# Optimization experiments

Hardware: AMD Instinct MI355X
Metric: run time of the kernel (lower is better)

The kernel has to match this reference:

```python
import jax, jax.numpy as jnp
import numpy as np

KAPPA = 5  # kNN neighbors per node (module hardcodes kappas = [5]*B, topk of KAPPA+2)


def build_graph(inputs):
    """Vectorized equivalent of get_graph(): returns flat (src, dst, edge_weight)
    over the B*S node space. Filtered kNN edges (dst < 2) are masked via weight 0,
    which is mathematically identical to removing them (gcn_norm uses edge weights)."""
    B, S, _ = inputs.shape
    diff = inputs[:, :, None, :] - inputs[:, None, :, :]            # [B,S,S,2]
    deltas = jnp.sqrt(jnp.sum(diff * diff, axis=-1))                # torch.cdist
    eye = jnp.eye(S, dtype=bool)
    d = jnp.where(eye[None], jnp.inf, deltas)                       # fill_diagonal_(inf)
    nodes = jnp.arange(2, S, dtype=jnp.int32)                       # non-depot nodes
    # depot edges: 0 -> i  and  i -> 1  for i in [2, S)
    src_dep = jnp.concatenate([jnp.zeros(S - 2, jnp.int32), nodes])
    dst_dep = jnp.concatenate([nodes, jnp.ones(S - 2, jnp.int32)])
    # kNN edges: 7 nearest per non-depot node (diag=inf so i never selected)
    _, idx = jax.lax.top_k(-d[:, 2:, :], KAPPA + 2)                 # [B, S-2, 7]
    src_knn = jnp.broadcast_to(nodes[:, None], (S - 2, KAPPA + 2)).reshape(-1)
    dst_knn = idx.reshape(B, -1).astype(jnp.int32)                  # [B, 7*(S-2)]
    mask_knn = (dst_knn >= 2).astype(jnp.float32)                   # drop depot dsts
    src = jnp.concatenate([jnp.broadcast_to(src_dep[None], (B, src_dep.shape[0])), jnp.broadcast_to(src_knn[None], (B, src_knn.shape[0]))], axis=1)
    dst = jnp.concatenate([jnp.broadcast_to(dst_dep[None], (B, dst_dep.shape[0])), dst_knn], axis=1)
    ew = jnp.concatenate([jnp.ones((B, dst_dep.shape[0]), jnp.float32), mask_knn], axis=1)
    offs = (jnp.arange(B, dtype=jnp.int32) * S)[:, None]            # batch node offset
    return (src + offs).reshape(-1), (dst + offs).reshape(-1), ew.reshape(-1)


def gcn_conv(x, src, dst, norm, self_norm, W, b, N):
    h = x @ W                                                       # GCNConv linear
    agg = jax.ops.segment_sum(h[src] * norm[:, None], dst, num_segments=N)
    agg = agg + h * self_norm[:, None]                              # self-loop term
    return agg + b


def gnn_forward(x, src, dst, ew, W0, b0, W1, b1, W2, b2):
    N = x.shape[0]
    deg = jax.ops.segment_sum(ew, dst, num_segments=N) + 1.0        # +1 self-loop
    dinv = 1.0 / jnp.sqrt(deg)
    norm = dinv[src] * dinv[dst] * ew                               # sym gcn_norm
    self_norm = dinv * dinv
    h = jax.nn.relu(gcn_conv(x, src, dst, norm, self_norm, W0, b0, N))
    h = jax.nn.relu(gcn_conv(h, src, dst, norm, self_norm, W1, b1, N))
    return gcn_conv(h, src, dst, norm, self_norm, W2, b2, N)


def setup_inputs() -> dict:
    B, S, D, H = 64, 1000, 128, 512
    key = jax.random.key(0)
    ks = jax.random.split(key, 12)
    sc = lambda fan_in: 1.0 / np.sqrt(fan_in)
    return {
        "inputs": jax.random.uniform(ks[0], (B, S, 2), jnp.float32),
        "scor": jax.random.uniform(ks[1], (B, S, 1), jnp.float32),
        "Wc": jax.random.normal(ks[2], (2, D), jnp.float32) * sc(2),
        "bc": jax.random.normal(ks[3], (D,), jnp.float32) * 0.01,
        "Ws": jax.random.normal(ks[4], (1, D), jnp.float32) * sc(1),
        "bs": jax.random.normal(ks[5], (D,), jnp.float32) * 0.01,
        "W0": jax.random.normal(ks[6], (D, H), jnp.float32) * sc(D),
        "b0": jnp.zeros((H,), jnp.float32),
        "W1": jax.random.normal(ks[8], (H, H), jnp.float32) * sc(H),
        "b1": jnp.zeros((H,), jnp.float32),
        "W2": jax.random.normal(ks[10], (H, D), jnp.float32) * sc(H),
        "b2": jnp.zeros((D,), jnp.float32),
    }


def reference(inputs, scor, Wc, bc, Ws, bs, W0, b0, W1, b1, W2, b2):
    B, S, _ = inputs.shape
    src, dst, ew = build_graph(inputs)
    x = (inputs @ Wc + bc) + (scor @ Ws + bs)                       # embedded_data
    x = x.reshape(B * S, -1)
    out = gnn_forward(x, src, dst, ew, W0, b0, W1, b1, W2, b2)
    return out.reshape(B, S, -1)
```

## Files before the change

kernel.cpp:

```cpp
#include <hip/hip_runtime.h>

typedef unsigned short u16;
typedef unsigned int u32;
typedef unsigned long long u64;
using short8 = __attribute__((ext_vector_type(8))) short;
using f32x4  = __attribute__((ext_vector_type(4))) float;

constexpr int Bb = 64, Ss = 1000, Dd = 128, Hh = 512;
constexpr int NN = Bb * Ss;
constexpr int NSRC = Ss - 2;

__device__ __forceinline__ float bf2f(u16 h) {
    u32 u = ((u32)h) << 16;
    return __builtin_bit_cast(float, u);
}
__device__ __forceinline__ u16 f2bf(float v) {
    u32 u = __builtin_bit_cast(u32, v);
    u32 r = (u + 0x7FFFu + ((u >> 16) & 1u)) >> 16;
    return (u16)r;
}
__device__ __forceinline__ float4 bf4(ushort4 v) {
    float4 r;
    r.x = bf2f(v.x); r.y = bf2f(v.y); r.z = bf2f(v.z); r.w = bf2f(v.w);
    return r;
}
__device__ __forceinline__ void gl_lds16(const void* g, void* l) {
    __builtin_amdgcn_global_load_lds(
        (const __attribute__((address_space(1))) void*)g,
        (__attribute__((address_space(3))) void*)l, 16, 0, 0);
}
__device__ __forceinline__ void acc8(float (&a)[8], uint4 v, float w) {
    u32 c[4] = {v.x, v.y, v.z, v.w};
#pragma unroll
    for (int k = 0; k < 4; ++k) {
        float lo = __builtin_bit_cast(float, c[k] << 16);
        float hi = __builtin_bit_cast(float, c[k] & 0xFFFF0000u);
        a[2 * k]     += lo * w;
        a[2 * k + 1] += hi * w;
    }
}
__device__ __forceinline__ void acc2(float (&a)[2], u32 v, float w) {
    float lo = __builtin_bit_cast(float, v << 16);
    float hi = __builtin_bit_cast(float, v & 0xFFFF0000u);
    a[0] += lo * w;
    a[1] += hi * w;
}
__device__ __forceinline__ void unp8(float (&a)[8], uint4 v) {
    u32 c[4] = {v.x, v.y, v.z, v.w};
#pragma unroll
    for (int k = 0; k < 4; ++k) {
        a[2 * k]     = __builtin_bit_cast(float, c[k] << 16);
        a[2 * k + 1] = __builtin_bit_cast(float, c[k] & 0xFFFF0000u);
    }
}

__device__ __forceinline__ u64 umin64(u64 a, u64 b) { return a < b ? a : b; }
__device__ __forceinline__ u64 umax64(u64 a, u64 b) { return a < b ? b : a; }

__device__ __forceinline__ void ins8u(u64 (&bd)[8], u64 v) {
#pragma unroll
    for (int k = 7; k >= 1; --k)
        bd[k] = umin64(umax64(v, bd[k - 1]), bd[k]);
    bd[0] = umin64(v, bd[0]);
}

__device__ __forceinline__ void merge8(u64 (&a)[8], int mask) {
    u64 b[8];
#pragma unroll
    for (int k = 0; k < 8; ++k)
        b[k] = __shfl_xor((unsigned long long)a[k], mask);
    u64 m[8];
#pragma unroll
    for (int k = 0; k < 8; ++k) m[k] = umin64(a[k], b[7 - k]);
#pragma unroll
    for (int k = 0; k < 4; ++k) {
        u64 lo = umin64(m[k], m[k + 4]), hi = umax64(m[k], m[k + 4]);
        m[k] = lo; m[k + 4] = hi;
    }
#pragma unroll
    for (int base = 0; base < 8; base += 4)
#pragma unroll
        for (int k = 0; k < 2; ++k) {
            u64 lo = umin64(m[base + k], m[base + k + 2]);
            u64 hi = umax64(m[base + k], m[base + k + 2]);
            m[base + k] = lo; m[base + k + 2] = hi;
        }
#pragma unroll
    for (int base = 0; base < 8; base += 2) {
        u64 lo = umin64(m[base], m[base + 1]), hi = umax64(m[base], m[base + 1]);
        m[base] = lo; m[base + 1] = hi;
    }
#pragma unroll
    for (int k = 0; k < 8; ++k) a[k] = m[k];
}

__global__ __launch_bounds__(256) void knn_bin_kernel(const float* __restrict__ inputs,
                                                      float2* __restrict__ gsxy,
                                                      u16* __restrict__ gsid,
                                                      int* __restrict__ gcst) {
    __shared__ float px[Ss], py[Ss];
    __shared__ int hist[256];
    __shared__ int cur[256];
    int b = blockIdx.x;
    int tid = threadIdx.x;
    const float* base = inputs + (size_t)b * Ss * 2;
    for (int t = tid; t < Ss; t += 256) { px[t] = base[2 * t]; py[t] = base[2 * t + 1]; }
    hist[tid] = 0;
    __syncthreads();
    for (int t = tid; t < Ss; t += 256) {
        int cx = min(15, (int)(px[t] * 16.0f));
        int cy = min(15, (int)(py[t] * 16.0f));
        atomicAdd(&hist[cy * 16 + cx], 1);
    }
    __syncthreads();
    int cnt = hist[tid];
    for (int s = 1; s < 256; s <<= 1) {
        int u = (tid >= s) ? hist[tid - s] : 0;
        __syncthreads();
        hist[tid] += u;
        __syncthreads();
    }
    int st = hist[tid] - cnt;
    cur[tid] = st;
    gcst[b * 260 + tid] = st;
    if (tid == 0) gcst[b * 260 + 256] = Ss;
    __syncthreads();
    for (int t = tid; t < Ss; t += 256) {
        float x = px[t], y = py[t];
        int cx = min(15, (int)(x * 16.0f));
        int cy = min(15, (int)(y * 16.0f));
        int p = atomicAdd(&cur[cy * 16 + cx], 1);
        gsxy[b * 1000 + p] = make_float2(x, y);
        gsid[b * 1000 + p] = (u16)t;
    }
}

__global__ __launch_bounds__(256) void knn_query_kernel(const float* __restrict__ inputs,
                                                        const float2* __restrict__ gsxy,
                                                        const u16* __restrict__ gsid,
                                                        const int* __restrict__ gcst,
                                                        u16* __restrict__ knn,
                                                        int* __restrict__ indeg) {
    __shared__ float2 sxy[Ss];
    __shared__ u16 sid[Ss];
    __shared__ int cst[257];
    int b = blockIdx.x;
    int tid = threadIdx.x;
    for (int t = tid; t < Ss; t += 256) { sxy[t] = gsxy[b * 1000 + t]; sid[t] = gsid[b * 1000 + t]; }
    for (int t = tid; t < 257; t += 256) cst[t] = gcst[b * 260 + t];
    __syncthreads();

    int sub = tid & 7;
    int g = tid >> 3;
    int i = 2 + blockIdx.y * 32 + g;
    if (i >= Ss) return;

    float x = inputs[(size_t)b * 2000 + 2 * i];
    float y = inputs[(size_t)b * 2000 + 2 * i + 1];
    int cx = min(15, (int)(x * 16.0f));
    int cy = min(15, (int)(y * 16.0f));
    const float INF = __builtin_inff();
    constexpr float h = 0.0625f;

    u64 bd[8];
    int w = 1;
    for (;;) {
#pragma unroll
        for (int k = 0; k < 8; ++k) bd[k] = ~0ULL;
        int x0 = max(0, cx - w), x1 = min(15, cx + w);
        int y0 = max(0, cy - w), y1 = min(15, cy + w);
        for (int cyy = y0; cyy <= y1; ++cyy) {
            int p0 = cst[cyy * 16 + x0];
            int p1 = cst[cyy * 16 + x1 + 1];
            for (int p = p0 + sub; p < p1; p += 8) {
                float2 q = sxy[p];
                int j = sid[p];
                float dx = __fsub_rn(x, q.x);
                float dy = __fsub_rn(y, q.y);
                float d2 = __fadd_rn(__fmul_rn(dx, dx), __fmul_rn(dy, dy));
                float d = __fsqrt_rn(d2);
                u64 key = (((u64)__builtin_bit_cast(u32, d)) << 32) | (u32)j;
                key = (j == i) ? ~0ULL : key;
                ins8u(bd, key);
            }
        }
        merge8(bd, 1); merge8(bd, 2); merge8(bd, 4);
        float d7 = __builtin_bit_cast(float, (u32)(bd[6] >> 32));
        float bL = (x0 > 0)  ? (x - (float)x0 * h) : INF;
        float bR = (x1 < 15) ? ((float)(x1 + 1) * h - x) : INF;
        float bB = (y0 > 0)  ? (y - (float)y0 * h) : INF;
        float bT = (y1 < 15) ? ((float)(y1 + 1) * h - y) : INF;
        float bound = fminf(fminf(bL, bR), fminf(bB, bT));
        if (d7 <= bound - 2e-6f || w >= 16) break;
        ++w;
    }

    if (sub == 0) {
        u16* kp = knn + ((size_t)b * NSRC + (i - 2)) * 7;
#pragma unroll
        for (int k = 0; k < 7; ++k) {
            int j = (int)(u32)bd[k];
            kp[k] = (u16)j;
            if (j >= 2) atomicAdd(&indeg[b * Ss + j], 1);
        }
    }
}

__global__ __launch_bounds__(1024) void scan1_kernel(const int* __restrict__ indeg,
                                                     int* __restrict__ offs,
                                                     int* __restrict__ bsum,
                                                     float* __restrict__ dinv) {
    __shared__ int sh[1024];
    int t = threadIdx.x;
    int idx = blockIdx.x * 1024 + t;
    int v = (idx < NN) ? indeg[idx] : 0;
    sh[t] = v;
    __syncthreads();
    for (int off = 1; off < 1024; off <<= 1) {
        int u = (t >= off) ? sh[t - off] : 0;
        __syncthreads();
        sh[t] += u;
        __syncthreads();
    }
    if (idx < NN) {
        offs[idx] = sh[t] - v;
        int ii = idx % Ss;
        float deg = (ii == 0) ? 1.0f : (ii == 1) ? (float)(Ss - 1) : (float)(v + 2);
        dinv[idx] = 1.0f / __fsqrt_rn(deg);
    }
    if (t == 1023) bsum[blockIdx.x] = sh[1023];
}

__global__ void scan2_kernel(int* __restrict__ bsum) {
    if (threadIdx.x == 0) {
        int run = 0;
        for (int k = 0; k < 63; ++k) { int v = bsum[k]; bsum[k] = run; run += v; }
        bsum[63] = run;
    }
}

__global__ __launch_bounds__(1024) void scan3_kernel(int* __restrict__ offs,
                                                     const int* __restrict__ bsum) {
    int idx = blockIdx.x * 1024 + threadIdx.x;
    if (idx < NN) offs[idx] += bsum[blockIdx.x];
    if (idx == 0) offs[NN] = bsum[63];
}

__global__ __launch_bounds__(256) void fill_rev_kernel(const u16* __restrict__ knn,
                                                       const int* __restrict__ offs,
                                                       int* __restrict__ cursor,
                                                       u16* __restrict__ rev) {
    if (threadIdx.x >= 250) return;
    int b = blockIdx.x;
    int i = 2 + blockIdx.y * 250 + threadIdx.x;
    if (i >= Ss) return;
    const u16* kp = knn + ((size_t)b * NSRC + (i - 2)) * 7;
#pragma unroll
    for (int k = 0; k < 7; ++k) {
        int d = kp[k];
        if (d >= 2) {
            int n = b * Ss + d;
            int p = atomicAdd(&cursor[n], 1);
            rev[offs[n] + p] = (u16)i;
        }
    }
}

__global__ __launch_bounds__(512) void fuse0_kernel(const float* __restrict__ Wc,
                                                    const float* __restrict__ bc,
                                                    const float* __restrict__ Ws,
                                                    const float* __restrict__ bs,
                                                    const float* __restrict__ W0,
                                                    float* __restrict__ A) {
    int h = threadIdx.x;
    float a0 = 0.f, a1 = 0.f, a2 = 0.f, a3 = 0.f;
    for (int c = 0; c < Dd; ++c) {
        float w = W0[c * Hh + h];
        a0 += Wc[c] * w;
        a1 += Wc[Dd + c] * w;
        a2 += Ws[c] * w;
        a3 += (bc[c] + bs[c]) * w;
    }
    A[h] = a0; A[Hh + h] = a1; A[2 * Hh + h] = a2; A[3 * Hh + h] = a3;
}

__global__ __launch_bounds__(1024) void agg_e_kernel(const float* __restrict__ inputs,
                                                     const float* __restrict__ scor,
                                                     const float* __restrict__ dinv,
                                                     const int* __restrict__ offs,
                                                     const int* __restrict__ indeg,
                                                     const u16* __restrict__ rev,
                                                     float4* __restrict__ ve) {
    __shared__ float se0[Ss], se1[Ss], se2[Ss], sdv[Ss];
    __shared__ float4 depw[16];
    int b = blockIdx.x;
    int tid = threadIdx.x;
    int nb = b * Ss;
    const float* base = inputs + (size_t)nb * 2;
    for (int t = tid; t < Ss; t += 1024) {
        se0[t] = base[2 * t];
        se1[t] = base[2 * t + 1];
        se2[t] = scor[nb + t];
        sdv[t] = dinv[nb + t];
    }
    __syncthreads();

    float4 dep = {0.f, 0.f, 0.f, 0.f};
    for (int r = tid; r < Ss; r += 1024) {
        if (r >= 2) {
            float w = sdv[r];
            dep.x += se0[r] * w; dep.y += se1[r] * w;
            dep.z += se2[r] * w; dep.w += w;
        }
    }
#pragma unroll
    for (int m = 1; m < 64; m <<= 1) {
        dep.x += __shfl_xor(dep.x, m);
        dep.y += __shfl_xor(dep.y, m);
        dep.z += __shfl_xor(dep.z, m);
        dep.w += __shfl_xor(dep.w, m);
    }
    if ((tid & 63) == 0) depw[tid >> 6] = dep;
    __syncthreads();

    int i = tid;
    if (i >= Ss) return;
    float dn = sdv[i], sn = dn * dn;
    float4 acc = {0.f, 0.f, 0.f, 0.f};
    if (i >= 2) {
        int n = nb + i;
        int cnt = indeg[n], o = offs[n];
        float w0 = sdv[0];
        acc.x = se0[0] * w0; acc.y = se1[0] * w0;
        acc.z = se2[0] * w0; acc.w = w0;
        for (int e = 0; e < cnt; ++e) {
            int s = rev[o + e];
            float w = sdv[s];
            acc.x += se0[s] * w; acc.y += se1[s] * w;
            acc.z += se2[s] * w; acc.w += w;
        }
    } else if (i == 1) {
        float4 t = {0.f, 0.f, 0.f, 0.f};
#pragma unroll
        for (int k = 0; k < 16; ++k) {
            t.x += depw[k].x; t.y += depw[k].y;
            t.z += depw[k].z; t.w += depw[k].w;
        }
        acc = t;
    }
    float4 v;
    v.x = acc.x * dn + se0[i] * sn;
    v.y = acc.y * dn + se1[i] * sn;
    v.z = acc.z * dn + se2[i] * sn;
    v.w = acc.w * dn + sn;
    ve[nb + i] = v;
}

__global__ __launch_bounds__(256) void expand512p_kernel(const float4* __restrict__ ve,
                                                         const float* __restrict__ dinv,
                                                         const float* __restrict__ A,
                                                         const float* __restrict__ bias,
                                                         u16* __restrict__ X,
                                                         float* __restrict__ sxp) {
    __shared__ float4 sve[250];
    __shared__ float  sdv[250];
    __shared__ float  sred[8][256];
    int bx = blockIdx.x;
    int g = bx >> 1, cg = bx & 1;
    int b = blockIdx.y;
    int n0 = g * 250;
    int nb = b * Ss;
    int tid = threadIdx.x;
    int c32 = tid & 31, slice = tid >> 5;
    int ch = cg * 256 + c32 * 8;
    for (int t = tid; t < 250; t += 256) {
        sve[t] = ve[nb + n0 + t];
        sdv[t] = dinv[nb + n0 + t];
    }
    __syncthreads();

    float A0[8], A1[8], A2[8], A3[8], BZ[8];
#pragma unroll
    for (int j = 0; j < 8; ++j) {
        A0[j] = A[ch + j];
        A1[j] = A[Hh + ch + j];
        A2[j] = A[2 * Hh + ch + j];
        A3[j] = A[3 * Hh + ch + j];
        BZ[j] = bias[ch + j];
    }
    float acc[8] = {};
    for (int t = slice; t < 250; t += 8) {
        int n = n0 + t;
        float4 v = sve[t];
        float dw = (n >= 2) ? sdv[t] : 0.f;
        u32 ow[4];
#pragma unroll
        for (int j = 0; j < 4; ++j) {
            float z0 = fmaxf(v.x * A0[2 * j]     + v.y * A1[2 * j]     + v.z * A2[2 * j]     + v.w * A3[2 * j]     + BZ[2 * j],     0.f);
            float z1 = fmaxf(v.x * A0[2 * j + 1] + v.y * A1[2 * j + 1] + v.z * A2[2 * j + 1] + v.w * A3[2 * j + 1] + BZ[2 * j + 1], 0.f);
            u16 h0 = f2bf(z0), h1 = f2bf(z1);
            ow[j] = (u32)h0 | ((u32)h1 << 16);
            acc[2 * j]     += dw * bf2f(h0);
            acc[2 * j + 1] += dw * bf2f(h1);
        }
        uint4 o = {ow[0], ow[1], ow[2], ow[3]};
        *(uint4*)(X + (size_t)(nb + n) * Hh + ch) = o;
    }
#pragma unroll
    for (int j = 0; j < 8; ++j) sred[slice][c32 * 8 + j] = acc[j];
    __syncthreads();
    if (slice == 0) {
#pragma unroll
        for (int j = 0; j < 8; ++j) {
            float s = 0.f;
#pragma unroll
            for (int sl = 0; sl < 8; ++sl) s += sred[sl][c32 * 8 + j];
            sxp[((size_t)b * 4 + g) * Hh + ch + j] = s;
        }
    }
}

__global__ __launch_bounds__(512) void sxk_kernel(const float* __restrict__ sxp,
                                                  const float* __restrict__ W1,
                                                  float* __restrict__ depp) {
    __shared__ float sx[64];
    int kc = blockIdx.x;
    int b  = blockIdx.y;
    int t  = threadIdx.x;
    if (t < 64) {
        int k = kc * 64 + t;
        float s = 0.f;
#pragma unroll
        for (int g = 0; g < 4; ++g) s += sxp[((size_t)b * 4 + g) * Hh + k];
        sx[t] = s;
    }
    __syncthreads();
    float a = 0.f;
#pragma unroll 8
    for (int kk = 0; kk < 64; ++kk)
        a += sx[kk] * W1[(size_t)(kc * 64 + kk) * Hh + t];
    depp[((size_t)kc * Bb + b) * Hh + t] = a;
}

__global__ __launch_bounds__(512) void sxred_kernel(const float* __restrict__ depp,
                                                    float* __restrict__ depf) {
    int b = blockIdx.x, t = threadIdx.x;
    float s = 0.f;
#pragma unroll
    for (int kc = 0; kc < 8; ++kc)
        s += depp[((size_t)kc * Bb + b) * Hh + t];
    depf[(size_t)b * Hh + t] = s;
}

__global__ void transp_kernel(const float* __restrict__ src,
                              u16* __restrict__ dst, int R, int C) {
    int gid = blockIdx.x * 256 + threadIdx.x;
    if (gid >= R * C) return;
    int r = gid / C, c = gid - r * C;
    dst[c * R + r] = f2bf(src[gid]);
}

__global__ __launch_bounds__(256) void gemm_kernel(const u16* __restrict__ A,
                                                   const u16* __restrict__ W,
                                                   u16* __restrict__ Y,
                                                   int K, int Ncols,
                                                   int nyb, int nxb) {
    __shared__ __align__(16) u16 lA[128][64];
    __shared__ __align__(16) u16 lW[128][64];

    int grp = blockIdx.x / (8 * nxb);
    int rem = blockIdx.x - grp * (8 * nxb);
    int xcd = rem & 7;
    int xb  = rem >> 3;
    int yb  = grp * 8 + xcd;
    if (yb >= nyb) return;

    int row0 = yb * 128;
    int col0 = xb * 128;
    int tid = threadIdx.x;
    int lane = tid & 63, wid = tid >> 6;
    int wm = (wid >> 1) * 64, wn = (wid & 1) * 64;
    int lanelo = lane & 15, quad = lane >> 4;

    int lrow = lane >> 3;
    int lslot = lane & 7;

    f32x4 acc[4][4] = {};

    for (int k0 = 0; k0 < K; k0 += 64) {
#pragma unroll
        for (int t = 0; t < 4; ++t) {
            int chunk = t * 4 + wid;
            int row = chunk * 8 + lrow;
            int sc = lslot ^ (row & 7);
            gl_lds16(A + (size_t)(row0 + row) * K + k0 + sc * 8, &lA[chunk * 8][0]);
        }
#pragma unroll
        for (int t = 0; t < 4; ++t) {
            int chunk = t * 4 + wid;
            int row = chunk * 8 + lrow;
            int sc = lslot ^ (row & 7);
            gl_lds16(W + (size_t)(col0 + row) * K + k0 + sc * 8, &lW[chunk * 8][0]);
        }
        __syncthreads();

#pragma unroll
        for (int kk = 0; kk < 64; kk += 32) {
            short8 af[4], bw[4];
            int cbb = (kk >> 3) + quad;
#pragma unroll
            for (int mt = 0; mt < 4; ++mt) {
                int r = wm + mt * 16 + lanelo;
                af[mt] = *(const short8*)&lA[r][((cbb ^ (r & 7))) * 8];
            }
#pragma unroll
            for (int nt = 0; nt < 4; ++nt) {
                int r = wn + nt * 16 + lanelo;
                bw[nt] = *(const short8*)&lW[r][((cbb ^ (r & 7))) * 8];
            }
#pragma unroll
            for (int mt = 0; mt < 4; ++mt)
#pragma unroll
                for (int nt = 0; nt < 4; ++nt)
                    acc[mt][nt] = __builtin_amdgcn_mfma_f32_16x16x32_bf16(
                        af[mt], bw[nt], acc[mt][nt], 0, 0, 0);
        }
        __syncthreads();
    }

#pragma unroll
    for (int mt = 0; mt < 4; ++mt)
#pragma unroll
        for (int nt = 0; nt < 4; ++nt)
#pragma unroll
            for (int r = 0; r < 4; ++r) {
                int row = row0 + wm + mt * 16 + quad * 4 + r;
                int col = col0 + wn + nt * 16 + lanelo;
                Y[(size_t)row * Ncols + col] = f2bf(acc[mt][nt][r]);
            }
}

__global__ __launch_bounds__(1024) void dep1_kernel(const u16* __restrict__ y,
                                                    const float* __restrict__ dinv,
                                                    float* __restrict__ dq,
                                                    int M) {
    int b = blockIdx.x;
    int qq = blockIdx.y;
    int co = blockIdx.z * 128;
    int tid = threadIdx.x;
    int c4 = tid & 31;
    int es = tid >> 5;
    int j0 = 2 + qq * 250;
    int j1 = j0 + 250; if (j1 > Ss) j1 = Ss;
    const u16* yb = y + (size_t)b * Ss * M + co + c4 * 4;
    const float* dv = dinv + b * Ss;
    float a0 = 0.f, a1 = 0.f, a2 = 0.f, a3 = 0.f;
    for (int j = j0 + es; j < j1; j += 32) {
        float w = dv[j];
        float4 u = bf4(*(const ushort4*)(yb + (size_t)j * M));
        a0 += u.x * w; a1 += u.y * w; a2 += u.z * w; a3 += u.w * w;
    }
    __shared__ float4 red[1024];
    float4 mv; mv.x = a0; mv.y = a1; mv.z = a2; mv.w = a3;
    red[tid] = mv;
    __syncthreads();
#pragma unroll
    for (int s = 16; s > 0; s >>= 1) {
        if (es < s) {
            float4 o = red[tid + (s << 5)];
            float4 m = red[tid];
            m.x += o.x; m.y += o.y; m.z += o.z; m.w += o.w;
            red[tid] = m;
        }
        __syncthreads();
    }
    if (es == 0)
        *(float4*)(dq + ((size_t)qq * Bb + b) * M + co + c4 * 4) = red[c4];
}

__global__ __launch_bounds__(256) void aggw512_kernel(const u16* __restrict__ y,
                                                      const float* __restrict__ dinv,
                                                      const int* __restrict__ offs,
                                                      const int* __restrict__ indeg,
                                                      const u16* __restrict__ rev,
                                                      const float* __restrict__ bias,
                                                      const float* __restrict__ dep1,
                                                      u16* __restrict__ oX) {
    int tid = threadIdx.x;
    int wv = tid >> 6, lane = tid & 63;
    int bx = blockIdx.x;
    int b = (bx & 7) + 8 * (bx / 2000);
    int i = ((bx >> 3) % 250) * 4 + wv;
    int nb = b * Ss;
    int n = nb + i;
    const u16* yB = y + (size_t)nb * 512 + lane * 8;

    float acc[8] = {};
    if (i >= 2) {
        int cnt = indeg[n], o = offs[n];
        int rv = 0; float rw = 0.f;
        if (lane < 16 && lane < cnt) { rv = rev[o + lane]; rw = dinv[nb + rv]; }
        float w0 = dinv[nb];
        uint4 v0 = *(const uint4*)yB;
        acc8(acc, v0, w0);
        int cl = cnt < 16 ? cnt : 16;
        int e = 0;
        for (; e + 4 <= cl; e += 4) {
            int   s0 = __shfl(rv, e),     s1 = __shfl(rv, e + 1);
            int   s2 = __shfl(rv, e + 2), s3 = __shfl(rv, e + 3);
            float w_0 = __shfl(rw, e),     w_1 = __shfl(rw, e + 1);
            float w_2 = __shfl(rw, e + 2), w_3 = __shfl(rw, e + 3);
            uint4 u0 = *(const uint4*)(yB + (size_t)s0 * 512);
            uint4 u1 = *(const uint4*)(yB + (size_t)s1 * 512);
            uint4 u2 = *(const uint4*)(yB + (size_t)s2 * 512);
            uint4 u3 = *(const uint4*)(yB + (size_t)s3 * 512);
            acc8(acc, u0, w_0); acc8(acc, u1, w_1);
            acc8(acc, u2, w_2); acc8(acc, u3, w_3);
        }
        for (; e < cl; ++e) {
            int s = __shfl(rv, e); float ww = __shfl(rw, e);
            uint4 u = *(const uint4*)(yB + (size_t)s * 512);
            acc8(acc, u, ww);
        }
        for (; e < cnt; ++e) {
            int s = rev[o + e]; float ww = dinv[nb + s];
            uint4 u = *(const uint4*)(yB + (size_t)s * 512);
            acc8(acc, u, ww);
        }
    } else if (i == 1) {
        const float* dp = dep1 + (size_t)b * 512 + lane * 8;
        float4 v0 = *(const float4*)dp;
        float4 v1 = *(const float4*)(dp + 4);
        acc[0] = v0.x; acc[1] = v0.y; acc[2] = v0.z; acc[3] = v0.w;
        acc[4] = v1.x; acc[5] = v1.y; acc[6] = v1.z; acc[7] = v1.w;
    }
    float dn = dinv[n], sn = dn * dn;
    float s8[8];
    unp8(s8, *(const uint4*)(yB + (size_t)i * 512));
    float4 bl = *(const float4*)(bias + lane * 8);
    float4 bh = *(const float4*)(bias + lane * 8 + 4);
    float bz[8] = {bl.x, bl.y, bl.z, bl.w, bh.x, bh.y, bh.z, bh.w};
    u32 ow[4];
#pragma unroll
    for (int k = 0; k < 4; ++k) {
        float z0 = acc[2 * k]     * dn + s8[2 * k]     * sn + bz[2 * k];
        float z1 = acc[2 * k + 1] * dn + s8[2 * k + 1] * sn + bz[2 * k + 1];
        ow[k] = (u32)f2bf(fmaxf(z0, 0.f)) | ((u32)f2bf(fmaxf(z1, 0.f)) << 16);
    }
    uint4 ov = {ow[0], ow[1], ow[2], ow[3]};
    *(uint4*)(oX + (size_t)n * 512 + lane * 8) = ov;
}

__global__ __launch_bounds__(256) void aggwf128_kernel(const u16* __restrict__ y,
                                                       const float* __restrict__ dinv,
                                                       const int* __restrict__ offs,
                                                       const int* __restrict__ indeg,
                                                       const u16* __restrict__ rev,
                                                       const float* __restrict__ bias,
                                                       const float* __restrict__ dep1,
                                                       float* __restrict__ out) {
    int tid = threadIdx.x;
    int wv = tid >> 6, lane = tid & 63;
    int bx = blockIdx.x;
    int b = (bx & 7) + 8 * (bx / 2000);
    int i = ((bx >> 3) % 250) * 4 + wv;
    int nb = b * Ss;
    int n = nb + i;
    const u16* yB = y + (size_t)nb * 128 + lane * 2;

    float acc[2] = {};
    if (i >= 2) {
        int cnt = indeg[n], o = offs[n];
        int rv = 0; float rw = 0.f;
        if (lane < 16 && lane < cnt) { rv = rev[o + lane]; rw = dinv[nb + rv]; }
        float w0 = dinv[nb];
        acc2(acc, *(const u32*)yB, w0);
        int cl = cnt < 16 ? cnt : 16;
        int e = 0;
        for (; e + 4 <= cl; e += 4) {
            int   s0 = __shfl(rv, e),     s1 = __shfl(rv, e + 1);
            int   s2 = __shfl(rv, e + 2), s3 = __shfl(rv, e + 3);
            float w_0 = __shfl(rw, e),     w_1 = __shfl(rw, e + 1);
            float w_2 = __shfl(rw, e + 2), w_3 = __shfl(rw, e + 3);
            u32 u0 = *(const u32*)(yB + (size_t)s0 * 128);
            u32 u1 = *(const u32*)(yB + (size_t)s1 * 128);
            u32 u2 = *(const u32*)(yB + (size_t)s2 * 128);
            u32 u3 = *(const u32*)(yB + (size_t)s3 * 128);
            acc2(acc, u0, w_0); acc2(acc, u1, w_1);
            acc2(acc, u2, w_2); acc2(acc, u3, w_3);
        }
        for (; e < cl; ++e) {
            int s = __shfl(rv, e); float ww = __shfl(rw, e);
            acc2(acc, *(const u32*)(yB + (size_t)s * 128), ww);
        }
        for (; e < cnt; ++e) {
            int s = rev[o + e]; float ww = dinv[nb + s];
            acc2(acc, *(const u32*)(yB + (size_t)s * 128), ww);
        }
    } else if (i == 1) {
        const float* dp = dep1 + (size_t)b * 128 + lane * 2;
#pragma unroll
        for (int qq = 0; qq < 4; ++qq) {
            float2 v = *(const float2*)(dp + (size_t)qq * Bb * 128);
            acc[0] += v.x; acc[1] += v.y;
        }
    }
    float dn = dinv[n], sn = dn * dn;
    u32 sv = *(const u32*)(yB + (size_t)i * 128);
    float s0 = __builtin_bit_cast(float, sv << 16);
    float s1 = __builtin_bit_cast(float, sv & 0xFFFF0000u);
    float2 bz = *(const float2*)(bias + lane * 2);
    float2 z;
    z.x = acc[0] * dn + s0 * sn + bz.x;
    z.y = acc[1] * dn + s1 * sn + bz.y;
    *(float2*)(out + (size_t)n * 128 + lane * 2) = z;
}

constexpr size_t O_INDEG  = 0;
constexpr size_t O_CURSOR = 256000;
constexpr size_t O_OFFS   = 512000;
constexpr size_t O_DINV   = 768256;
constexpr size_t O_KNN    = 1024256;
constexpr size_t O_REV    = 1918080;
constexpr size_t O_AMAT   = 2811904;
constexpr size_t O_WT1    = 2942976;
constexpr size_t O_WT2    = 3467264;
constexpr size_t O_X      = 3598336;
constexpr size_t O_Y      = 69134336;
constexpr size_t O_SXP    = 134670336;
constexpr size_t O_DEPF   = 135194624;
constexpr size_t O_BSUM   = 135325696;
constexpr size_t O_GSXY   = O_X;
constexpr size_t O_GSID   = O_X + 512000;
constexpr size_t O_GCST   = O_X + 640000;
constexpr size_t O_VE     = O_Y;
constexpr size_t O_DEPP   = O_Y + 4194304;

extern "C" void kernel_launch(void* const* d_in, const int* in_sizes, int n_in,
                              void* d_out, int out_size, void* d_ws, size_t ws_size,
                              hipStream_t stream) {
    const float* inputs = (const float*)d_in[0];
    const float* scor   = (const float*)d_in[1];
    const float* Wc     = (const float*)d_in[2];
    const float* bc     = (const float*)d_in[3];
    const float* Ws     = (const float*)d_in[4];
    const float* bs     = (const float*)d_in[5];
    const float* W0     = (const float*)d_in[6];
    const float* b0     = (const float*)d_in[7];
    const float* W1     = (const float*)d_in[8];
    const float* b1     = (const float*)d_in[9];
    const float* W2     = (const float*)d_in[10];
    const float* b2     = (const float*)d_in[11];

    char* w = (char*)d_ws;
    int*    indeg  = (int*)(w + O_INDEG);
    int*    cursor = (int*)(w + O_CURSOR);
    int*    offs   = (int*)(w + O_OFFS);
    float*  dinv   = (float*)(w + O_DINV);
    u16*    knn    = (u16*)(w + O_KNN);
    u16*    rev    = (u16*)(w + O_REV);
    float*  amat   = (float*)(w + O_AMAT);
    u16*    wt1    = (u16*)(w + O_WT1);
    u16*    wt2    = (u16*)(w + O_WT2);
    u16*    xbf    = (u16*)(w + O_X);
    u16*    ybf    = (u16*)(w + O_Y);
    float*  sxp    = (float*)(w + O_SXP);
    float*  depf   = (float*)(w + O_DEPF);
    float*  depp   = (float*)(w + O_DEPP);
    int*    bsum   = (int*)(w + O_BSUM);
    float2* gsxy   = (float2*)(w + O_GSXY);
    u16*    gsid   = (u16*)(w + O_GSID);
    int*    gcst   = (int*)(w + O_GCST);
    float4* ve     = (float4*)(w + O_VE);

    hipMemsetAsync(w + O_INDEG, 0, 512000, stream);

    knn_bin_kernel<<<Bb, 256, 0, stream>>>(inputs, gsxy, gsid, gcst);
    knn_query_kernel<<<dim3(Bb, 32), 256, 0, stream>>>(inputs, gsxy, gsid, gcst, knn, indeg);
    scan1_kernel<<<63, 1024, 0, stream>>>(indeg, offs, bsum, dinv);
    scan2_kernel<<<1, 64, 0, stream>>>(bsum);
    scan3_kernel<<<63, 1024, 0, stream>>>(offs, bsum);
    fill_rev_kernel<<<dim3(Bb, 4), 256, 0, stream>>>(knn, offs, cursor, rev);

    fuse0_kernel<<<1, 512, 0, stream>>>(Wc, bc, Ws, bs, W0, amat);
    transp_kernel<<<(Hh * Hh + 255) / 256, 256, 0, stream>>>(W1, wt1, Hh, Hh);
    transp_kernel<<<(Hh * Dd + 255) / 256, 256, 0, stream>>>(W2, wt2, Hh, Dd);

    agg_e_kernel<<<Bb, 1024, 0, stream>>>(inputs, scor, dinv, offs, indeg, rev, ve);
    expand512p_kernel<<<dim3(8, Bb), 256, 0, stream>>>(ve, dinv, amat, b0, xbf, sxp);
    sxk_kernel<<<dim3(8, Bb), 512, 0, stream>>>(sxp, W1, depp);
    sxred_kernel<<<Bb, 512, 0, stream>>>(depp, depf);
    gemm_kernel<<<63 * 32, 256, 0, stream>>>(xbf, wt1, ybf, Hh, Hh, 500, 4);
    aggw512_kernel<<<NN / 4, 256, 0, stream>>>(ybf, dinv, offs, indeg, rev, b1, depf, xbf);
    gemm_kernel<<<63 * 8, 256, 0, stream>>>(xbf, wt2, ybf, Hh, Dd, 500, 1);
    dep1_kernel<<<dim3(Bb, 4, 1), 1024, 0, stream>>>(ybf, dinv, depf, Dd);
    aggwf128_kernel<<<NN / 4, 256, 0, stream>>>(ybf, dinv, offs, indeg, rev, b2, depf, (float*)d_out);
}
```

Before: 308.9 us.

## Fold scan2 into scan3, merge prep kernels, enlarge GEMM tile to 256 rows

Removes the single-thread scan2 launch by having every scan3 block compute its own prefix of the block sums with wavefront shuffles. Merges fuse0 and the two weight-transpose kernels into one prep kernel to cut launch count. Doubles the GEMM M-tile to 256 rows with 512 threads per block, which raises reuse of the weight tile but halves the number of blocks. The wave-to-tile mapping in the unshown compute part must match the new 8-wave layout.

Result: no change. 310.3 us (+0.5%).

```diff
diff --git a/kernel.cpp b/kernel.cpp
--- a/kernel.cpp
+++ b/kernel.cpp
@@ -231,19 +231,25 @@
     if (t == 1023) bsum[blockIdx.x] = sh[1023];
 }
 
-__global__ void scan2_kernel(int* __restrict__ bsum) {
-    if (threadIdx.x == 0) {
-        int run = 0;
-        for (int k = 0; k < 63; ++k) { int v = bsum[k]; bsum[k] = run; run += v; }
-        bsum[63] = run;
-    }
-}
-
 __global__ __launch_bounds__(1024) void scan3_kernel(int* __restrict__ offs,
                                                      const int* __restrict__ bsum) {
-    int idx = blockIdx.x * 1024 + threadIdx.x;
-    if (idx < NN) offs[idx] += bsum[blockIdx.x];
-    if (idx == 0) offs[NN] = bsum[63];
+    __shared__ int spre, stot;
+    int t = threadIdx.x;
+    if (t < 64) {
+        int v = (t < 63) ? bsum[t] : 0;
+        int pre = (t < (int)blockIdx.x) ? v : 0;
+        int tot = v;
+#pragma unroll
+        for (int m = 1; m < 64; m <<= 1) {
+            pre += __shfl_xor(pre, m);
+            tot += __shfl_xor(tot, m);
+        }
+        if (t == 0) { spre = pre; stot = tot; }
+    }
+    __syncthreads();
+    int idx = blockIdx.x * 1024 + t;
+    if (idx < NN) offs[idx] += spre;
+    if (idx == 0) offs[NN] = stot;
 }
 
 __global__ __launch_bounds__(256) void fill_rev_kernel(const u16* __restrict__ knn,
@@ -266,22 +272,38 @@
     }
 }
 
-__global__ __launch_bounds__(512) void fuse0_kernel(const float* __restrict__ Wc,
-                                                    const float* __restrict__ bc,
-                                                    const float* __restrict__ Ws,
-                                                    const float* __restrict__ bs,
-                                                    const float* __restrict__ W0,
-                                                    float* __restrict__ A) {
-    int h = threadIdx.x;
-    float a0 = 0.f, a1 = 0.f, a2 = 0.f, a3 = 0.f;
-    for (int c = 0; c < Dd; ++c) {
-        float w = W0[c * Hh + h];
-        a0 += Wc[c] * w;
-        a1 += Wc[Dd + c] * w;
-        a2 += Ws[c] * w;
-        a3 += (bc[c] + bs[c]) * w;
-    }
-    A[h] = a0; A[Hh + h] = a1; A[2 * Hh + h] = a2; A[3 * Hh + h] = a3;
+__global__ __launch_bounds__(256) void prep_kernel(const float* __restrict__ Wc,
+                                                   const float* __restrict__ bc,
+                                                   const float* __restrict__ Ws,
+                                                   const float* __restrict__ bs,
+                                                   const float* __restrict__ W0,
+                                                   const float* __restrict__ W1,
+                                                   const float* __restrict__ W2,
+                                                   float* __restrict__ A,
+                                                   u16* __restrict__ wt1,
+                                                   u16* __restrict__ wt2) {
+    int bid = blockIdx.x;
+    int tid = threadIdx.x;
+    if (bid < 1024) {
+        int gid = bid * 256 + tid;
+        int r = gid >> 9, c = gid & 511;
+        wt1[(size_t)c * 512 + r] = f2bf(W1[gid]);
+    } else if (bid < 1024 + 256) {
+        int gid = (bid - 1024) * 256 + tid;
+        int r = gid >> 7, c = gid & 127;
+        wt2[(size_t)c * 512 + r] = f2bf(W2[gid]);
+    } else {
+        int h = (bid - 1280) * 256 + tid;
+        float a0 = 0.f, a1 = 0.f, a2 = 0.f, a3 = 0.f;
+        for (int c = 0; c < Dd; ++c) {
+            float w = W0[c * Hh + h];
+            a0 += Wc[c] * w;
+            a1 += Wc[Dd + c] * w;
+            a2 += Ws[c] * w;
+            a3 += (bc[c] + bs[c]) * w;
+        }
+        A[h] = a0; A[Hh + h] = a1; A[2 * Hh + h] = a2; A[3 * Hh + h] = a3;
+    }
 }
 
 __global__ __launch_bounds__(1024) void agg_e_kernel(const float* __restrict__ inputs,
@@ -452,20 +474,12 @@
     depf[(size_t)b * Hh + t] = s;
 }
 
-__global__ void transp_kernel(const float* __restrict__ src,
-                              u16* __restrict__ dst, int R, int C) {
-    int gid = blockIdx.x * 256 + threadIdx.x;
-    if (gid >= R * C) return;
-    int r = gid / C, c = gid - r * C;
-    dst[c * R + r] = f2bf(src[gid]);
-}
-
-__global__ __launch_bounds__(256) void gemm_kernel(const u16* __restrict__ A,
+__global__ __launch_bounds__(512) void gemm_kernel(const u16* __restrict__ A,
                                                    const u16* __restrict__ W,
                                                    u16* __restrict__ Y,
                                                    int K, int Ncols,
                                                    int nyb, int nxb) {
-    __shared__ __align__(16) u16 lA[128][64];
+    __shared__ __align__(16) u16 lA[256][64];
     __shared__ __align__(16) u16 lW[128][64];
 
     int grp = blockIdx.x / (8 * nxb);
@@ -475,7 +489,7 @@
     int yb  = grp * 8 + xcd;
     if (yb >= nyb) return;
 
-    int row0 = yb * 128;
+    int row0 = yb * 256;
     int col0 = xb * 128;
     int tid = threadIdx.x;
     int lane = tid & 63, wid = tid >> 6;
@@ -490,14 +504,14 @@
     for (int k0 = 0; k0 < K; k0 += 64) {
 #pragma unroll
         for (int t = 0; t < 4; ++t) {
-            int chunk = t * 4 + wid;
+            int chunk = t * 8 + wid;
             int row = chunk * 8 + lrow;
             int sc = lslot ^ (row & 7);
             gl_lds16(A + (size_t)(row0 + row) * K + k0 + sc * 8, &lA[chunk * 8][0]);
         }
 #pragma unroll
-        for (int t = 0; t < 4; ++t) {
-            int chunk = t * 4 + wid;
+        for (int t = 0; t < 2; ++t) {
+            int chunk = t * 8 + wid;
             int row = chunk * 8 + lrow;
             int sc = lslot ^ (row & 7);
             gl_lds16(W + (size_t)(col0 + row) * K + k0 + sc * 8, &lW[chunk * 8][0]);
@@ -778,21 +792,18 @@
     knn_bin_kernel<<<Bb, 256, 0, stream>>>(inputs, gsxy, gsid, gcst);
     knn_query_kernel<<<dim3(Bb, 32), 256, 0, stream>>>(inputs, gsxy, gsid, gcst, knn, indeg);
     scan1_kernel<<<63, 1024, 0, stream>>>(indeg, offs, bsum, dinv);
-    scan2_kernel<<<1, 64, 0, stream>>>(bsum);
     scan3_kernel<<<63, 1024, 0, stream>>>(offs, bsum);
     fill_rev_kernel<<<dim3(Bb, 4), 256, 0, stream>>>(knn, offs, cursor, rev);
 
-    fuse0_kernel<<<1, 512, 0, stream>>>(Wc, bc, Ws, bs, W0, amat);
-    transp_kernel<<<(Hh * Hh + 255) / 256, 256, 0, stream>>>(W1, wt1, Hh, Hh);
-    transp_kernel<<<(Hh * Dd + 255) / 256, 256, 0, stream>>>(W2, wt2, Hh, Dd);
+    prep_kernel<<<1282, 256, 0, stream>>>(Wc, bc, Ws, bs, W0, W1, W2, amat, wt1, wt2);
 
     agg_e_kernel<<<Bb, 1024, 0, stream>>>(inputs, scor, dinv, offs, indeg, rev, ve);
     expand512p_kernel<<<dim3(8, Bb), 256, 0, stream>>>(ve, dinv, amat, b0, xbf, sxp);
     sxk_kernel<<<dim3(8, Bb), 512, 0, stream>>>(sxp, W1, depp);
     sxred_kernel<<<Bb, 512, 0, stream>>>(depp, depf);
-    gemm_kernel<<<63 * 32, 256, 0, stream>>>(xbf, wt1, ybf, Hh, Hh, 500, 4);
+    gemm_kernel<<<32 * 8 * 4, 512, 0, stream>>>(xbf, wt1, ybf, Hh, Hh, 250, 4);
     aggw512_kernel<<<NN / 4, 256, 0, stream>>>(ybf, dinv, offs, indeg, rev, b1, depf, xbf);
-    gemm_kernel<<<63 * 8, 256, 0, stream>>>(xbf, wt2, ybf, Hh, Dd, 500, 1);
+    gemm_kernel<<<32 * 8, 512, 0, stream>>>(xbf, wt2, ybf, Hh, Dd, 250, 1);
     dep1_kernel<<<dim3(Bb, 4, 1), 1024, 0, stream>>>(ybf, dinv, depf, Dd);
     aggwf128_kernel<<<NN / 4, 256, 0, stream>>>(ybf, dinv, offs, indeg, rev, b2, depf, (float*)d_out);
 }
```
